# Kernel optimization log

Measured on AMD Instinct MI355X. Metric: run time of the kernel, lower is better.

Reference implementation:

```python
import jax, jax.numpy as jnp
import numpy as np

N_NODES = 50000
N_EDGES = 600000
D_IN = 128
D_HID = 1024
D_OUT = 128


def setup_inputs() -> dict:
    key = jax.random.key(0)
    ks = jax.random.split(key, 8)
    feat = jax.random.normal(ks[0], (N_NODES, D_IN), dtype=jnp.float32)
    edge_feat = jax.random.normal(ks[1], (N_EDGES, D_IN), dtype=jnp.float32)
    src = jax.random.randint(ks[2], (N_EDGES,), 0, N_NODES, dtype=jnp.int32)
    dst = jax.random.randint(ks[3], (N_EDGES,), 0, N_NODES, dtype=jnp.int32)
    W1 = jax.random.normal(ks[4], (D_IN, D_HID), dtype=jnp.float32) * (1.0 / np.sqrt(D_IN))
    b1 = jnp.zeros((D_HID,), dtype=jnp.float32)
    W2 = jax.random.normal(ks[5], (D_HID, D_OUT), dtype=jnp.float32) * (1.0 / np.sqrt(D_HID))
    b2 = jnp.zeros((D_OUT,), dtype=jnp.float32)
    return {"feat": feat, "edge_feat": edge_feat, "src": src, "dst": dst,
            "W1": W1, "b1": b1, "W2": W2, "b2": b2}


def reference(feat, edge_feat, src, dst, W1, b1, W2, b2):
    # DGL u_add_e: message m_e = h_src(e) + e_feat(e)   [E, D_IN]
    messages = feat[src] + edge_feat
    # reduce sum over incoming edges at each destination node -> [N, D_IN]
    h = jax.ops.segment_sum(messages, dst, num_segments=N_NODES)
    # 2-layer MLP
    h = jax.nn.relu(h @ W1 + b1)
    return h @ W2 + b2
```

## Files before the change

### kernel.cpp

```cpp
#include <hip/hip_runtime.h>
#include <hip/hip_bf16.h>

#define N_NODES 50000
#define N_EDGES 600000
#define D_IN    128
#define D_HID   1024
#define D_OUT   128

#define WS_H      0
#define WS_EID    12800000
#define WS_OFF    15200000
#define WS_CURSOR 15400016
#define WS_DEG    15600016
#define WS_BSUM   15800016
#define WS_W1T    15801040
#define WS_W2T    16063184

typedef short bf16x8 __attribute__((ext_vector_type(8)));
typedef float f32x4  __attribute__((ext_vector_type(4)));

__global__ __launch_bounds__(256) void hist_kernel(
    const int* __restrict__ dst, int* __restrict__ deg)
{
    int e = blockIdx.x * blockDim.x + threadIdx.x;
    if (e < N_EDGES) atomicAdd(&deg[dst[e]], 1);
}

__global__ __launch_bounds__(256) void scan1_kernel(
    const int* __restrict__ deg, int* __restrict__ bsum)
{
    __shared__ int red[256];
    int t = threadIdx.x;
    int idx = blockIdx.x * 256 + t;
    red[t] = (idx < N_NODES) ? deg[idx] : 0;
    __syncthreads();
    for (int s = 128; s > 0; s >>= 1) {
        if (t < s) red[t] += red[t + s];
        __syncthreads();
    }
    if (t == 0) bsum[blockIdx.x] = red[0];
}

#define SCAN_NB 196
__global__ __launch_bounds__(256) void scan2_kernel(
    int* __restrict__ bsum, int* __restrict__ off)
{
    __shared__ int sh[256];
    int t = threadIdx.x;
    int v = (t < SCAN_NB) ? bsum[t] : 0;
    sh[t] = v;
    __syncthreads();
    for (int ofs = 1; ofs < 256; ofs <<= 1) {
        int u = (t >= ofs) ? sh[t - ofs] : 0;
        __syncthreads();
        sh[t] += u;
        __syncthreads();
    }
    if (t < SCAN_NB) bsum[t] = sh[t] - v;
    if (t == 255) off[N_NODES] = sh[255];
}

__global__ __launch_bounds__(256) void scan3_kernel(
    const int* __restrict__ deg, const int* __restrict__ bsum,
    int* __restrict__ off, int* __restrict__ cursor)
{
    __shared__ int sh[256];
    int t = threadIdx.x;
    int idx = blockIdx.x * 256 + t;
    int v = (idx < N_NODES) ? deg[idx] : 0;
    sh[t] = v;
    __syncthreads();
    for (int ofs = 1; ofs < 256; ofs <<= 1) {
        int u = (t >= ofs) ? sh[t - ofs] : 0;
        __syncthreads();
        sh[t] += u;
        __syncthreads();
    }
    if (idx < N_NODES) {
        int ex = bsum[blockIdx.x] + sh[t] - v;
        off[idx] = ex;
        cursor[idx] = ex;
    }
}

__global__ __launch_bounds__(256) void fill_kernel(
    const int* __restrict__ dst, int* __restrict__ cursor, int* __restrict__ eid)
{
    int e = blockIdx.x * blockDim.x + threadIdx.x;
    if (e < N_EDGES) {
        int pos = atomicAdd(&cursor[dst[e]], 1);
        eid[pos] = e;
    }
}

__global__ __launch_bounds__(256) void transpose_cvt_kernel(
    const float* __restrict__ in, __hip_bfloat16* __restrict__ outp,
    int rows, int cols)
{
    __shared__ float tile[32][33];
    int c0 = blockIdx.x * 32, r0 = blockIdx.y * 32;
    int tx = threadIdx.x & 31, ty = threadIdx.x >> 5;
    #pragma unroll
    for (int i = 0; i < 32; i += 8) {
        int r = r0 + ty + i, c = c0 + tx;
        tile[ty + i][tx] = (r < rows && c < cols) ? in[(size_t)r * cols + c] : 0.f;
    }
    __syncthreads();
    #pragma unroll
    for (int i = 0; i < 32; i += 8) {
        int c = c0 + ty + i, r = r0 + tx;
        if (r < rows && c < cols)
            outp[(size_t)c * rows + r] = __float2bfloat16(tile[tx][ty + i]);
    }
}

__global__ __launch_bounds__(256) void gather_kernel(
    const float* __restrict__ feat,
    const float* __restrict__ edge_feat,
    const int*   __restrict__ src,
    const int*   __restrict__ eid,
    const int*   __restrict__ off,
    __hip_bfloat16* __restrict__ hbf)
{
    const int wv   = __builtin_amdgcn_readfirstlane(threadIdx.x >> 6);
    const int lane = threadIdx.x & 63;
    const int n = blockIdx.x * 4 + wv;
    if (n >= N_NODES) return;

    int i   = __builtin_amdgcn_readfirstlane(off[n]);
    int end = __builtin_amdgcn_readfirstlane(off[n + 1]);

    float2 a0 = make_float2(0.f, 0.f), a1 = a0, a2 = a0, a3 = a0;

    for (; i + 3 < end; i += 4) {
        int e0 = __builtin_amdgcn_readfirstlane(eid[i]);
        int e1 = __builtin_amdgcn_readfirstlane(eid[i + 1]);
        int e2 = __builtin_amdgcn_readfirstlane(eid[i + 2]);
        int e3 = __builtin_amdgcn_readfirstlane(eid[i + 3]);
        int s0 = __builtin_amdgcn_readfirstlane(src[e0]);
        int s1 = __builtin_amdgcn_readfirstlane(src[e1]);
        int s2 = __builtin_amdgcn_readfirstlane(src[e2]);
        int s3 = __builtin_amdgcn_readfirstlane(src[e3]);
        float2 f0 = ((const float2*)(edge_feat + (size_t)e0 * D_IN))[lane];
        float2 g0 = ((const float2*)(feat      + (size_t)s0 * D_IN))[lane];
        float2 f1 = ((const float2*)(edge_feat + (size_t)e1 * D_IN))[lane];
        float2 g1 = ((const float2*)(feat      + (size_t)s1 * D_IN))[lane];
        float2 f2 = ((const float2*)(edge_feat + (size_t)e2 * D_IN))[lane];
        float2 g2 = ((const float2*)(feat      + (size_t)s2 * D_IN))[lane];
        float2 f3 = ((const float2*)(edge_feat + (size_t)e3 * D_IN))[lane];
        float2 g3 = ((const float2*)(feat      + (size_t)s3 * D_IN))[lane];
        a0.x += f0.x + g0.x;  a0.y += f0.y + g0.y;
        a1.x += f1.x + g1.x;  a1.y += f1.y + g1.y;
        a2.x += f2.x + g2.x;  a2.y += f2.y + g2.y;
        a3.x += f3.x + g3.x;  a3.y += f3.y + g3.y;
    }
    for (; i < end; ++i) {
        int e = __builtin_amdgcn_readfirstlane(eid[i]);
        int s = __builtin_amdgcn_readfirstlane(src[e]);
        float2 f = ((const float2*)(edge_feat + (size_t)e * D_IN))[lane];
        float2 g = ((const float2*)(feat      + (size_t)s * D_IN))[lane];
        a0.x += f.x + g.x;  a0.y += f.y + g.y;
    }
    float sx = (a0.x + a1.x) + (a2.x + a3.x);
    float sy = (a0.y + a1.y) + (a2.y + a3.y);
    __hip_bfloat162 hv;
    hv.x = __float2bfloat16(sx);
    hv.y = __float2bfloat16(sy);
    ((__hip_bfloat162*)(hbf + (size_t)n * D_IN))[lane] = hv;
}

#define HS_STRIDE 136
#define QS_STRIDE 72

__global__ __launch_bounds__(256) void mlp_mfma_kernel(
    const __hip_bfloat16* __restrict__ hbf,
    const __hip_bfloat16* __restrict__ w1t,
    const float* __restrict__ b1,
    const __hip_bfloat16* __restrict__ w2t,
    const float* __restrict__ b2,
    float* __restrict__ out)
{
    __shared__ __align__(16) short h_s[64 * HS_STRIDE];
    __shared__ __align__(16) short q_s[64 * QS_STRIDE];

    const int t    = threadIdx.x;
    const int wv   = t >> 6;
    const int lane = t & 63;
    const int half = lane >> 4;
    const int lid  = lane & 15;
    const int nb   = blockIdx.x * 64;

    const short* hs  = (const short*)hbf;
    const short* w1s = (const short*)w1t;
    const short* w2s = (const short*)w2t;

    for (int u = t; u < 64 * 16; u += 256) {
        int r = u >> 4, c = u & 15;
        int row = nb + r;
        uint4 v = make_uint4(0u, 0u, 0u, 0u);
        if (row < N_NODES) v = ((const uint4*)(hs + (size_t)row * 128))[c];
        *(uint4*)&h_s[r * HS_STRIDE + c * 8] = v;
    }
    __syncthreads();

    bf16x8 afrag[4][4];
    #pragma unroll
    for (int mt = 0; mt < 4; ++mt)
        #pragma unroll
        for (int ks = 0; ks < 4; ++ks)
            afrag[mt][ks] = *(const bf16x8*)&h_s[(mt * 16 + lid) * HS_STRIDE + ks * 32 + half * 8];

    f32x4 acc[4][2];
    #pragma unroll
    for (int mt = 0; mt < 4; ++mt) {
        acc[mt][0] = f32x4{0.f, 0.f, 0.f, 0.f};
        acc[mt][1] = f32x4{0.f, 0.f, 0.f, 0.f};
    }

    const int ncol1 = wv * 16 + lid;

    for (int jb = 0; jb < D_HID; jb += 64) {
        float bias = b1[jb + ncol1];
        bf16x8 bfrag[4];
        #pragma unroll
        for (int ks = 0; ks < 4; ++ks)
            bfrag[ks] = *(const bf16x8*)&w1s[(size_t)(jb + ncol1) * 128 + ks * 32 + half * 8];

        f32x4 c1[4];
        #pragma unroll
        for (int mt = 0; mt < 4; ++mt) {
            f32x4 c = f32x4{bias, bias, bias, bias};
            #pragma unroll
            for (int ks = 0; ks < 4; ++ks)
                c = __builtin_amdgcn_mfma_f32_16x16x32_bf16(afrag[mt][ks], bfrag[ks], c, 0, 0, 0);
            c1[mt] = c;
        }

        __syncthreads();
        #pragma unroll
        for (int mt = 0; mt < 4; ++mt) {
            #pragma unroll
            for (int r = 0; r < 4; ++r) {
                float v = fmaxf(c1[mt][r], 0.f);
                __hip_bfloat16 bv = __float2bfloat16(v);
                q_s[(mt * 16 + half * 4 + r) * QS_STRIDE + wv * 16 + lid] = *(short*)&bv;
            }
        }
        __syncthreads();

        bf16x8 a2f[4][2];
        #pragma unroll
        for (int mt = 0; mt < 4; ++mt)
            #pragma unroll
            for (int ks = 0; ks < 2; ++ks)
                a2f[mt][ks] = *(const bf16x8*)&q_s[(mt * 16 + lid) * QS_STRIDE + ks * 32 + half * 8];

        #pragma unroll
        for (int nt = 0; nt < 2; ++nt) {
            #pragma unroll
            for (int ks = 0; ks < 2; ++ks) {
                bf16x8 b2f = *(const bf16x8*)&w2s[(size_t)(wv * 32 + nt * 16 + lid) * 1024 + jb + ks * 32 + half * 8];
                #pragma unroll
                for (int mt = 0; mt < 4; ++mt)
                    acc[mt][nt] = __builtin_amdgcn_mfma_f32_16x16x32_bf16(a2f[mt][ks], b2f, acc[mt][nt], 0, 0, 0);
            }
        }
    }

    #pragma unroll
    for (int nt = 0; nt < 2; ++nt) {
        int col = wv * 32 + nt * 16 + lid;
        float bv = b2[col];
        #pragma unroll
        for (int mt = 0; mt < 4; ++mt) {
            #pragma unroll
            for (int r = 0; r < 4; ++r) {
                int row = nb + mt * 16 + half * 4 + r;
                if (row < N_NODES)
                    out[(size_t)row * D_OUT + col] = acc[mt][nt][r] + bv;
            }
        }
    }
}

extern "C" void kernel_launch(void* const* d_in, const int* in_sizes, int n_in,
                              void* d_out, int out_size, void* d_ws, size_t ws_size,
                              hipStream_t stream) {
    const float* feat      = (const float*)d_in[0];
    const float* edge_feat = (const float*)d_in[1];
    const int*   src       = (const int*)d_in[2];
    const int*   dst       = (const int*)d_in[3];
    const float* W1        = (const float*)d_in[4];
    const float* b1        = (const float*)d_in[5];
    const float* W2        = (const float*)d_in[6];
    const float* b2        = (const float*)d_in[7];
    float* out = (float*)d_out;

    char* ws = (char*)d_ws;
    __hip_bfloat16* hbf    = (__hip_bfloat16*)(ws + WS_H);
    int*   eid    = (int*)(ws + WS_EID);
    int*   off    = (int*)(ws + WS_OFF);
    int*   cursor = (int*)(ws + WS_CURSOR);
    int*   deg    = (int*)(ws + WS_DEG);
    int*   bsum   = (int*)(ws + WS_BSUM);
    __hip_bfloat16* w1t = (__hip_bfloat16*)(ws + WS_W1T);
    __hip_bfloat16* w2t = (__hip_bfloat16*)(ws + WS_W2T);

    hipMemsetAsync(deg, 0, (size_t)N_NODES * sizeof(int), stream);

    hist_kernel<<<(N_EDGES + 255) / 256, 256, 0, stream>>>(dst, deg);
    scan1_kernel<<<SCAN_NB, 256, 0, stream>>>(deg, bsum);
    scan2_kernel<<<1, 256, 0, stream>>>(bsum, off);
    scan3_kernel<<<SCAN_NB, 256, 0, stream>>>(deg, bsum, off, cursor);
    fill_kernel<<<(N_EDGES + 255) / 256, 256, 0, stream>>>(dst, cursor, eid);

    transpose_cvt_kernel<<<dim3(1024 / 32, 128 / 32), 256, 0, stream>>>(W1, w1t, D_IN, D_HID);
    transpose_cvt_kernel<<<dim3(128 / 32, 1024 / 32), 256, 0, stream>>>(W2, w2t, D_HID, D_OUT);

    gather_kernel<<<(N_NODES + 3) / 4, 256, 0, stream>>>(feat, edge_feat, src, eid, off, hbf);

    mlp_mfma_kernel<<<(N_NODES + 63) / 64, 256, 0, stream>>>(hbf, w1t, b1, w2t, b2, out);
}
```

Before: 610.9 us.

## Fuse gather into MLP kernel and double-buffer hidden-layer LDS

```diff
diff --git a/kernel.cpp b/kernel.cpp
--- a/kernel.cpp
+++ b/kernel.cpp
@@ -7,7 +7,6 @@
 #define D_HID   1024
 #define D_OUT   128
 
-#define WS_H      0
 #define WS_EID    12800000
 #define WS_OFF    15200000
 #define WS_CURSOR 15400016
@@ -93,87 +92,43 @@
     }
 }
 
-__global__ __launch_bounds__(256) void transpose_cvt_kernel(
-    const float* __restrict__ in, __hip_bfloat16* __restrict__ outp,
-    int rows, int cols)
+__global__ __launch_bounds__(256) void transpose_cvt2_kernel(
+    const float* __restrict__ W1, __hip_bfloat16* __restrict__ w1t,
+    const float* __restrict__ W2, __hip_bfloat16* __restrict__ w2t)
 {
     __shared__ float tile[32][33];
-    int c0 = blockIdx.x * 32, r0 = blockIdx.y * 32;
+    int b = blockIdx.x;
+    const float* in;
+    __hip_bfloat16* outp;
+    int rows, cols, c0, r0;
+    if (b < 128) {
+        in = W1; outp = w1t; rows = D_IN; cols = D_HID;
+        c0 = (b & 31) * 32; r0 = (b >> 5) * 32;
+    } else {
+        int bb = b - 128;
+        in = W2; outp = w2t; rows = D_HID; cols = D_OUT;
+        c0 = (bb & 3) * 32; r0 = (bb >> 2) * 32;
+    }
     int tx = threadIdx.x & 31, ty = threadIdx.x >> 5;
     #pragma unroll
-    for (int i = 0; i < 32; i += 8) {
-        int r = r0 + ty + i, c = c0 + tx;
-        tile[ty + i][tx] = (r < rows && c < cols) ? in[(size_t)r * cols + c] : 0.f;
-    }
-    __syncthreads();
-    #pragma unroll
-    for (int i = 0; i < 32; i += 8) {
-        int c = c0 + ty + i, r = r0 + tx;
-        if (r < rows && c < cols)
-            outp[(size_t)c * rows + r] = __float2bfloat16(tile[tx][ty + i]);
-    }
-}
-
-__global__ __launch_bounds__(256) void gather_kernel(
+    for (int i = 0; i < 32; i += 8)
+        tile[ty + i][tx] = in[(size_t)(r0 + ty + i) * cols + (c0 + tx)];
+    __syncthreads();
+    #pragma unroll
+    for (int i = 0; i < 32; i += 8)
+        outp[(size_t)(c0 + ty + i) * rows + (r0 + tx)] =
+            __float2bfloat16(tile[tx][ty + i]);
+}
+
+#define HS_STRIDE 136
+#define QS_STRIDE 72
+
+__global__ __launch_bounds__(256) void fused_gnn_kernel(
     const float* __restrict__ feat,
     const float* __restrict__ edge_feat,
     const int*   __restrict__ src,
     const int*   __restrict__ eid,
     const int*   __restrict__ off,
-    __hip_bfloat16* __restrict__ hbf)
-{
-    const int wv   = __builtin_amdgcn_readfirstlane(threadIdx.x >> 6);
-    const int lane = threadIdx.x & 63;
-    const int n = blockIdx.x * 4 + wv;
-    if (n >= N_NODES) return;
-
-    int i   = __builtin_amdgcn_readfirstlane(off[n]);
-    int end = __builtin_amdgcn_readfirstlane(off[n + 1]);
-
-    float2 a0 = make_float2(0.f, 0.f), a1 = a0, a2 = a0, a3 = a0;
-
-    for (; i + 3 < end; i += 4) {
-        int e0 = __builtin_amdgcn_readfirstlane(eid[i]);
-        int e1 = __builtin_amdgcn_readfirstlane(eid[i + 1]);
-        int e2 = __builtin_amdgcn_readfirstlane(eid[i + 2]);
-        int e3 = __builtin_amdgcn_readfirstlane(eid[i + 3]);
-        int s0 = __builtin_amdgcn_readfirstlane(src[e0]);
-        int s1 = __builtin_amdgcn_readfirstlane(src[e1]);
-        int s2 = __builtin_amdgcn_readfirstlane(src[e2]);
-        int s3 = __builtin_amdgcn_readfirstlane(src[e3]);
-        float2 f0 = ((const float2*)(edge_feat + (size_t)e0 * D_IN))[lane];
-        float2 g0 = ((const float2*)(feat      + (size_t)s0 * D_IN))[lane];
-        float2 f1 = ((const float2*)(edge_feat + (size_t)e1 * D_IN))[lane];
-        float2 g1 = ((const float2*)(feat      + (size_t)s1 * D_IN))[lane];
-        float2 f2 = ((const float2*)(edge_feat + (size_t)e2 * D_IN))[lane];
-        float2 g2 = ((const float2*)(feat      + (size_t)s2 * D_IN))[lane];
-        float2 f3 = ((const float2*)(edge_feat + (size_t)e3 * D_IN))[lane];
-        float2 g3 = ((const float2*)(feat      + (size_t)s3 * D_IN))[lane];
-        a0.x += f0.x + g0.x;  a0.y += f0.y + g0.y;
-        a1.x += f1.x + g1.x;  a1.y += f1.y + g1.y;
-        a2.x += f2.x + g2.x;  a2.y += f2.y + g2.y;
-        a3.x += f3.x + g3.x;  a3.y += f3.y + g3.y;
-    }
-    for (; i < end; ++i) {
-        int e = __builtin_amdgcn_readfirstlane(eid[i]);
-        int s = __builtin_amdgcn_readfirstlane(src[e]);
-        float2 f = ((const float2*)(edge_feat + (size_t)e * D_IN))[lane];
-        float2 g = ((const float2*)(feat      + (size_t)s * D_IN))[lane];
-        a0.x += f.x + g.x;  a0.y += f.y + g.y;
-    }
-    float sx = (a0.x + a1.x) + (a2.x + a3.x);
-    float sy = (a0.y + a1.y) + (a2.y + a3.y);
-    __hip_bfloat162 hv;
-    hv.x = __float2bfloat16(sx);
-    hv.y = __float2bfloat16(sy);
-    ((__hip_bfloat162*)(hbf + (size_t)n * D_IN))[lane] = hv;
-}
-
-#define HS_STRIDE 136
-#define QS_STRIDE 72
-
-__global__ __launch_bounds__(256) void mlp_mfma_kernel(
-    const __hip_bfloat16* __restrict__ hbf,
     const __hip_bfloat16* __restrict__ w1t,
     const float* __restrict__ b1,
     const __hip_bfloat16* __restrict__ w2t,
@@ -181,7 +136,7 @@
     float* __restrict__ out)
 {
     __shared__ __align__(16) short h_s[64 * HS_STRIDE];
-    __shared__ __align__(16) short q_s[64 * QS_STRIDE];
+    __shared__ __align__(16) short q_s[2][64 * QS_STRIDE];
 
     const int t    = threadIdx.x;
     const int wv   = t >> 6;
@@ -190,16 +145,52 @@
     const int lid  = lane & 15;
     const int nb   = blockIdx.x * 64;
 
-    const short* hs  = (const short*)hbf;
     const short* w1s = (const short*)w1t;
     const short* w2s = (const short*)w2t;
 
-    for (int u = t; u < 64 * 16; u += 256) {
-        int r = u >> 4, c = u & 15;
-        int row = nb + r;
-        uint4 v = make_uint4(0u, 0u, 0u, 0u);
-        if (row < N_NODES) v = ((const uint4*)(hs + (size_t)row * 128))[c];
-        *(uint4*)&h_s[r * HS_STRIDE + c * 8] = v;
+    for (int j = 0; j < 16; ++j) {
+        const int r = wv * 16 + j;
+        const int n = nb + r;
+        float2 a0 = make_float2(0.f, 0.f), a1 = a0, a2 = a0, a3 = a0;
+        if (n < N_NODES) {
+            int i   = __builtin_amdgcn_readfirstlane(off[n]);
+            int end = __builtin_amdgcn_readfirstlane(off[n + 1]);
+            for (; i + 3 < end; i += 4) {
+                int e0 = __builtin_amdgcn_readfirstlane(eid[i]);
+                int e1 = __builtin_amdgcn_readfirstlane(eid[i + 1]);
+                int e2 = __builtin_amdgcn_readfirstlane(eid[i + 2]);
+                int e3 = __builtin_amdgcn_readfirstlane(eid[i + 3]);
+                int s0 = __builtin_amdgcn_readfirstlane(src[e0]);
+                int s1 = __builtin_amdgcn_readfirstlane(src[e1]);
+                int s2 = __builtin_amdgcn_readfirstlane(src[e2]);
+                int s3 = __builtin_amdgcn_readfirstlane(src[e3]);
+                float2 f0 = ((const float2*)(edge_feat + (size_t)e0 * D_IN))[lane];
+                float2 g0 = ((const float2*)(feat      + (size_t)s0 * D_IN))[lane];
+                float2 f1 = ((const float2*)(edge_feat + (size_t)e1 * D_IN))[lane];
+                float2 g1 = ((const float2*)(feat      + (size_t)s1 * D_IN))[lane];
+                float2 f2 = ((const float2*)(edge_feat + (size_t)e2 * D_IN))[lane];
+                float2 g2 = ((const float2*)(feat      + (size_t)s2 * D_IN))[lane];
+                float2 f3 = ((const float2*)(edge_feat + (size_t)e3 * D_IN))[lane];
+                float2 g3 = ((const float2*)(feat      + (size_t)s3 * D_IN))[lane];
+                a0.x += f0.x + g0.x;  a0.y += f0.y + g0.y;
+                a1.x += f1.x + g1.x;  a1.y += f1.y + g1.y;
+                a2.x += f2.x + g2.x;  a2.y += f2.y + g2.y;
+                a3.x += f3.x + g3.x;  a3.y += f3.y + g3.y;
+            }
+            for (; i < end; ++i) {
+                int e = __builtin_amdgcn_readfirstlane(eid[i]);
+                int s = __builtin_amdgcn_readfirstlane(src[e]);
+                float2 f = ((const float2*)(edge_feat + (size_t)e * D_IN))[lane];
+                float2 g = ((const float2*)(feat      + (size_t)s * D_IN))[lane];
+                a0.x += f.x + g.x;  a0.y += f.y + g.y;
+            }
+        }
+        float sx = (a0.x + a1.x) + (a2.x + a3.x);
+        float sy = (a0.y + a1.y) + (a2.y + a3.y);
+        __hip_bfloat162 hv;
+        hv.x = __float2bfloat16(sx);
+        hv.y = __float2bfloat16(sy);
+        *(__hip_bfloat162*)&h_s[r * HS_STRIDE + lane * 2] = hv;
     }
     __syncthreads();
 
@@ -219,7 +210,8 @@
 
     const int ncol1 = wv * 16 + lid;
 
-    for (int jb = 0; jb < D_HID; jb += 64) {
+    int pb = 0;
+    for (int jb = 0; jb < D_HID; jb += 64, pb ^= 1) {
         float bias = b1[jb + ncol1];
         bf16x8 bfrag[4];
         #pragma unroll
@@ -236,14 +228,13 @@
             c1[mt] = c;
         }
 
-        __syncthreads();
         #pragma unroll
         for (int mt = 0; mt < 4; ++mt) {
             #pragma unroll
             for (int r = 0; r < 4; ++r) {
                 float v = fmaxf(c1[mt][r], 0.f);
                 __hip_bfloat16 bv = __float2bfloat16(v);
-                q_s[(mt * 16 + half * 4 + r) * QS_STRIDE + wv * 16 + lid] = *(short*)&bv;
+                q_s[pb][(mt * 16 + half * 4 + r) * QS_STRIDE + wv * 16 + lid] = *(short*)&bv;
             }
         }
         __syncthreads();
@@ -253,7 +244,7 @@
         for (int mt = 0; mt < 4; ++mt)
             #pragma unroll
             for (int ks = 0; ks < 2; ++ks)
-                a2f[mt][ks] = *(const bf16x8*)&q_s[(mt * 16 + lid) * QS_STRIDE + ks * 32 + half * 8];
+                a2f[mt][ks] = *(const bf16x8*)&q_s[pb][(mt * 16 + lid) * QS_STRIDE + ks * 32 + half * 8];
 
         #pragma unroll
         for (int nt = 0; nt < 2; ++nt) {
@@ -297,7 +288,6 @@
     float* out = (float*)d_out;
 
     char* ws = (char*)d_ws;
-    __hip_bfloat16* hbf    = (__hip_bfloat16*)(ws + WS_H);
     int*   eid    = (int*)(ws + WS_EID);
     int*   off    = (int*)(ws + WS_OFF);
     int*   cursor = (int*)(ws + WS_CURSOR);
@@ -314,10 +304,8 @@
     scan3_kernel<<<SCAN_NB, 256, 0, stream>>>(deg, bsum, off, cursor);
     fill_kernel<<<(N_EDGES + 255) / 256, 256, 0, stream>>>(dst, cursor, eid);
 
-    transpose_cvt_kernel<<<dim3(1024 / 32, 128 / 32), 256, 0, stream>>>(W1, w1t, D_IN, D_HID);
-    transpose_cvt_kernel<<<dim3(128 / 32, 1024 / 32), 256, 0, stream>>>(W2, w2t, D_HID, D_OUT);
-
-    gather_kernel<<<(N_NODES + 3) / 4, 256, 0, stream>>>(feat, edge_feat, src, eid, off, hbf);
-
-    mlp_mfma_kernel<<<(N_NODES + 63) / 64, 256, 0, stream>>>(hbf, w1t, b1, w2t, b2, out);
-}
+    transpose_cvt2_kernel<<<256, 256, 0, stream>>>(W1, w1t, W2, w2t);
+
+    fused_gnn_kernel<<<(N_NODES + 63) / 64, 256, 0, stream>>>(
+        feat, edge_feat, src, eid, off, w1t, b1, w2t, b2, out);
+}
```

New measurement: 655.5 us. 7.3% more time.
